# Optimization experiments

Measured on AMD Instinct MI355X. Metric: run time of the kernel, lower is better.

## Reference

```python
import jax, jax.numpy as jnp
import numpy as np
import math

B, T, C, H, D = 2, 2048, 768, 12, 64


def _rms_norm(x):
    # torch F.rms_norm with eps=None -> finfo(dtype).eps, no learned weight
    eps = jnp.finfo(x.dtype).eps
    return x * jax.lax.rsqrt(jnp.mean(x * x, axis=-1, keepdims=True) + eps)


def _apply_rotary(x, cos, sin):
    # nanochat rotary: split head_dim into halves
    d = x.shape[-1] // 2
    x1, x2 = x[..., :d], x[..., d:]
    return jnp.concatenate([x1 * cos + x2 * sin, -x1 * sin + x2 * cos], axis=-1)


def setup_inputs() -> dict:
    key = jax.random.key(0)
    ks = jax.random.split(key, 8)
    s = 0.02
    x = jax.random.normal(ks[0], (B, T, C), jnp.float32)
    cos = jax.random.normal(ks[1], (1, T, 1, D // 2), jnp.float32)
    sin = jax.random.normal(ks[2], (1, T, 1, D // 2), jnp.float32)
    Wq = jax.random.normal(ks[3], (C, C), jnp.float32) * s
    Wk = jax.random.normal(ks[4], (C, C), jnp.float32) * s
    Wv = jax.random.normal(ks[5], (C, C), jnp.float32) * s
    Wo = jax.random.normal(ks[6], (C, C), jnp.float32) * s
    beta = jnp.ones((H,), jnp.float32) * 0.5
    return {"x": x, "cos": cos, "sin": sin, "Wq": Wq, "Wk": Wk, "Wv": Wv, "Wo": Wo, "beta": beta}


def reference(x, cos, sin, Wq, Wk, Wv, Wo, beta):
    b, t, c = x.shape
    h = beta.shape[0]
    d = c // h
    q = (x @ Wq.T).reshape(b, t, h, d)
    k = (x @ Wk.T).reshape(b, t, h, d)
    v = (x @ Wv.T).reshape(b, t, h, d)
    q = _rms_norm(_apply_rotary(q, cos, sin)).transpose(0, 2, 1, 3)  # (B,H,T,D)
    k = _rms_norm(_apply_rotary(k, cos, sin)).transpose(0, 2, 1, 3)
    v = v.transpose(0, 2, 1, 3)
    # phase coherence: mean over RoPE frequencies of cos(position_diff * theta)
    pos = jnp.arange(t, dtype=jnp.float32)
    theta = 10000.0 ** (-jnp.arange(0, d, 2, dtype=jnp.float32) / d)  # (D/2,)
    pdiff = pos[None, :] - pos[:, None]  # (T,T); cos is even so orientation is irrelevant
    coh_base = jnp.mean(jnp.cos(pdiff[:, :, None] * theta), axis=-1)  # (T,T)
    coherence = 1.0 + beta[None, :, None, None] * coh_base[None, None, :, :]  # (1,H,T,T)
    scores = jnp.einsum('bhqd,bhkd->bhqk', q, k) / math.sqrt(d)
    scores = scores * coherence
    w = jax.nn.softmax(scores, axis=-1)
    causal = jnp.tril(jnp.ones((t, t), dtype=bool))
    w = w * causal[None, None, :, :]
    w = w / (jnp.sum(w, axis=-1, keepdims=True) + 1e-8)
    y = jnp.einsum('bhqk,bhkd->bhqd', w, v)
    y = y.transpose(0, 2, 1, 3).reshape(b, t, c)
    return y @ Wo.T
```

## Files before the change

### kernel.cpp

```cpp
#include <hip/hip_runtime.h>
#include <hip/hip_bf16.h>
#include <math.h>

#define B_ 2
#define T_ 2048
#define C_ 768
#define H_ 12
#define D_ 64

typedef __attribute__((ext_vector_type(8))) short short8;
typedef __attribute__((ext_vector_type(4))) float f32x4;
typedef __attribute__((ext_vector_type(16))) float f32x16;

template <bool V> struct BoolC { static constexpr bool value = V; };

#define SBAR() do { asm volatile("" ::: "memory"); __builtin_amdgcn_s_barrier(); asm volatile("" ::: "memory"); } while (0)
#define WAITVM(N) asm volatile("s_waitcnt vmcnt(" #N ")" ::: "memory")

__device__ inline unsigned short f2bf(float f) {
    unsigned int x = __float_as_uint(f);
    unsigned int r = x + 0x7FFFu + ((x >> 16) & 1u);
    return (unsigned short)(r >> 16);
}

__device__ __forceinline__ unsigned cvtpk(float lo, float hi) {
    unsigned r;
    asm("v_cvt_pk_bf16_f32 %0, %1, %2" : "=v"(r) : "v"(lo), "v"(hi));
    return r;
}

__device__ __forceinline__ void plswap(unsigned& a, unsigned& b) {
    asm volatile("v_permlane32_swap_b32 %0, %1" : "+v"(a), "+v"(b));
}

__device__ __forceinline__ void gll16(const void* g, void* l) {
    __builtin_amdgcn_global_load_lds(
        (const __attribute__((address_space(1))) unsigned int*)g,
        (__attribute__((address_space(3))) unsigned int*)l, 16, 0, 0);
}

__global__ __launch_bounds__(256) void convert_all_kernel(const float* __restrict__ x,
                                                          const float* __restrict__ Wq,
                                                          const float* __restrict__ Wk,
                                                          const float* __restrict__ Wv,
                                                          const float* __restrict__ Wo,
                                                          unsigned short* __restrict__ xb,
                                                          unsigned short* __restrict__ wqkv,
                                                          unsigned short* __restrict__ wob,
                                                          float* __restrict__ coh) {
    if (blockIdx.x >= 5376) {
        int dd = (blockIdx.x - 5376) * 256 + threadIdx.x;
        if (dd < T_) {
            float s = 0.f;
            for (int m = 0; m < 32; ++m) {
                float theta = powf(10000.f, -(float)m / 32.f);
                s += cosf((float)dd * theta);
            }
            coh[dd] = s * (1.f / 32.f);
        }
        return;
    }
    int i = blockIdx.x * 256 + threadIdx.x;
    float4 v;
    ushort4* d;
    if (i < 786432) {
        v = ((const float4*)x)[i];
        d = (ushort4*)xb + i;
    } else {
        int wI = i - 786432;
        int widx = wI / 147456;
        int off = wI - widx * 147456;
        const float* W = widx == 0 ? Wq : widx == 1 ? Wk : widx == 2 ? Wv : Wo;
        v = ((const float4*)W)[off];
        unsigned short* base = (widx == 3) ? wob : (wqkv + widx * 589824);
        d = (ushort4*)base + off;
    }
    ushort4 o;
    o.x = f2bf(v.x); o.y = f2bf(v.y); o.z = f2bf(v.z); o.w = f2bf(v.w);
    *d = o;
}

union QkvSmem {
    struct { unsigned short A[2][128][32]; unsigned short Bm[2][64][32]; } g;
    unsigned short tr[64][136];
};

__global__ __launch_bounds__(256, 4) void gemm_qkv_kernel(const unsigned short* __restrict__ xb,
                                                          const unsigned short* __restrict__ wqkv,
                                                          const float* __restrict__ cosb,
                                                          const float* __restrict__ sinb,
                                                          unsigned short* __restrict__ qbf,
                                                          unsigned short* __restrict__ kbf,
                                                          unsigned short* __restrict__ vt) {
    __shared__ QkvSmem sm;

    int bm = blockIdx.x, tn = blockIdx.y;
    int tid = threadIdx.x;
    int w = tid >> 6, lane = tid & 63;
    int rc = lane & 15, kg = lane >> 4;

    const unsigned short* ga = xb + (size_t)(bm * 128 + w * 32 + (lane >> 2)) * 768 + (lane & 3) * 8;
    const unsigned short* gb = wqkv + (size_t)(tn * 64 + w * 16 + (lane >> 2)) * 768 + (lane & 3) * 8;

    f32x4 acc[2][4];
    #pragma unroll
    for (int i = 0; i < 2; ++i)
        #pragma unroll
        for (int j = 0; j < 4; ++j) acc[i][j] = (f32x4){0.f, 0.f, 0.f, 0.f};

    auto stageg = [&](int buf, int k0) {
        gll16(ga + k0, &sm.g.A[buf][w * 32][0]);
        gll16(ga + k0 + 16 * 768, &sm.g.A[buf][w * 32 + 16][0]);
        gll16(gb + k0, &sm.g.Bm[buf][w * 16][0]);
    };
    auto comp = [&](int buf) {
        short8 aF[2], bF[4];
        #pragma unroll
        for (int ai = 0; ai < 2; ++ai) aF[ai] = *(const short8*)&sm.g.A[buf][w * 32 + ai * 16 + rc][kg * 8];
        #pragma unroll
        for (int bj = 0; bj < 4; ++bj) bF[bj] = *(const short8*)&sm.g.Bm[buf][bj * 16 + rc][kg * 8];
        __builtin_amdgcn_s_setprio(1);
        #pragma unroll
        for (int ai = 0; ai < 2; ++ai)
            #pragma unroll
            for (int bj = 0; bj < 4; ++bj)
                acc[ai][bj] = __builtin_amdgcn_mfma_f32_16x16x32_bf16(aF[ai], bF[bj], acc[ai][bj], 0, 0, 0);
        __builtin_amdgcn_s_setprio(0);
    };

    stageg(0, 0);
    __syncthreads();
    for (int kk = 0; kk < 23; ++kk) {
        stageg((kk + 1) & 1, (kk + 1) * 32);
        WAITVM(3);
        SBAR();
        comp(kk & 1);
        SBAR();
    }
    WAITVM(0);
    SBAR();
    comp(1);
    __syncthreads();

    int tensor = tn / 12;
    int h = tn % 12;

    if (tensor < 2) {
        float scale = tensor == 0 ? 0.125f : 1.0f;
        unsigned short* dst = (tensor == 0 ? qbf : kbf);
        #pragma unroll
        for (int ai = 0; ai < 2; ++ai) {
            #pragma unroll
            for (int rr = 0; rr < 4; ++rr) {
                int m = bm * 128 + w * 32 + ai * 16 + kg * 4 + rr;
                int b = m >> 11, t = m & 2047;
                float c0 = cosb[t * 32 + rc], c1 = cosb[t * 32 + 16 + rc];
                float s0 = sinb[t * 32 + rc], s1 = sinb[t * 32 + 16 + rc];
                float x0 = acc[ai][0][rr], x1 = acc[ai][1][rr];
                float x2 = acc[ai][2][rr], x3 = acc[ai][3][rr];
                float o0 = x0 * c0 + x2 * s0;
                float o1 = x1 * c1 + x3 * s1;
                float o2 = -x0 * s0 + x2 * c0;
                float o3 = -x1 * s1 + x3 * c1;
                float ss = o0 * o0 + o1 * o1 + o2 * o2 + o3 * o3;
                ss += __shfl_xor(ss, 1); ss += __shfl_xor(ss, 2);
                ss += __shfl_xor(ss, 4); ss += __shfl_xor(ss, 8);
                float rn = rsqrtf(ss * (1.f / 64.f) + 1.1920929e-07f) * scale;
                unsigned short* dp = dst + (((size_t)b * H_ + h) * T_ + t) * 64;
                dp[rc]      = f2bf(o0 * rn);
                dp[16 + rc] = f2bf(o1 * rn);
                dp[32 + rc] = f2bf(o2 * rn);
                dp[48 + rc] = f2bf(o3 * rn);
            }
        }
    } else {
        #pragma unroll
        for (int ai = 0; ai < 2; ++ai)
            #pragma unroll
            for (int bj = 0; bj < 4; ++bj)
                #pragma unroll
                for (int rr = 0; rr < 4; ++rr)
                    sm.tr[bj * 16 + rc][w * 32 + ai * 16 + kg * 4 + rr] = f2bf(acc[ai][bj][rr]);
        __syncthreads();
        int m0 = bm * 128;
        int b = m0 >> 11, t0 = m0 & 2047;
        int d = w * 16 + (lane >> 2);
        int tl = (lane & 3) * 32;
        unsigned short* gp = vt + (((size_t)b * H_ + h) * 64 + d) * T_ + t0 + tl;
        #pragma unroll
        for (int i = 0; i < 4; ++i)
            *(uint4*)(gp + i * 8) = *(const uint4*)&sm.tr[d][tl + i * 8];
    }
}

__global__ __launch_bounds__(256, 4) void gemm_out_kernel(const unsigned short* __restrict__ A,
                                                          const unsigned short* __restrict__ Bw,
                                                          float* __restrict__ C) {
    __shared__ unsigned short lA[2][64][32];
    __shared__ unsigned short lB[2][64][32];
    int bm = blockIdx.x, tn = blockIdx.y;
    int tid = threadIdx.x;
    int w = tid >> 6, lane = tid & 63;
    int rc = lane & 15, kg = lane >> 4;
    int wr = w >> 1, wc = w & 1;

    const unsigned short* ga = A + (size_t)(bm * 64 + w * 16 + (lane >> 2)) * 768 + (lane & 3) * 8;
    const unsigned short* gbB = Bw + (size_t)(tn * 64 + w * 16 + (lane >> 2)) * 768 + (lane & 3) * 8;

    f32x4 acc[2][2];
    #pragma unroll
    for (int i = 0; i < 2; ++i)
        #pragma unroll
        for (int j = 0; j < 2; ++j) acc[i][j] = (f32x4){0.f, 0.f, 0.f, 0.f};

    auto stageg = [&](int buf, int k0) {
        gll16(ga + k0, &lA[buf][w * 16][0]);
        gll16(gbB + k0, &lB[buf][w * 16][0]);
    };
    auto comp = [&](int buf) {
        short8 aF[2], bF[2];
        #pragma unroll
        for (int ai = 0; ai < 2; ++ai) aF[ai] = *(const short8*)&lA[buf][wr * 32 + ai * 16 + rc][kg * 8];
        #pragma unroll
        for (int bj = 0; bj < 2; ++bj) bF[bj] = *(const short8*)&lB[buf][wc * 32 + bj * 16 + rc][kg * 8];
        __builtin_amdgcn_s_setprio(1);
        #pragma unroll
        for (int ai = 0; ai < 2; ++ai)
            #pragma unroll
            for (int bj = 0; bj < 2; ++bj)
                acc[ai][bj] = __builtin_amdgcn_mfma_f32_16x16x32_bf16(aF[ai], bF[bj], acc[ai][bj], 0, 0, 0);
        __builtin_amdgcn_s_setprio(0);
    };

    stageg(0, 0);
    __syncthreads();
    for (int kk = 0; kk < 23; ++kk) {
        stageg((kk + 1) & 1, (kk + 1) * 32);
        WAITVM(2);
        SBAR();
        comp(kk & 1);
        SBAR();
    }
    WAITVM(0);
    SBAR();
    comp(1);

    #pragma unroll
    for (int ai = 0; ai < 2; ++ai)
        #pragma unroll
        for (int rr = 0; rr < 4; ++rr) {
            int m = bm * 64 + wr * 32 + ai * 16 + kg * 4 + rr;
            #pragma unroll
            for (int bj = 0; bj < 2; ++bj)
                C[(size_t)m * 768 + tn * 64 + wc * 32 + bj * 16 + rc] = acc[ai][bj][rr];
        }
}

__global__ __launch_bounds__(256, 4) void attn_flash_kernel(const unsigned short* __restrict__ qbf,
                                                            const unsigned short* __restrict__ kbf,
                                                            const unsigned short* __restrict__ vt,
                                                            const float* __restrict__ coh,
                                                            const float* __restrict__ beta,
                                                            unsigned short* __restrict__ yb) {
    __shared__ unsigned short kT[2][64][64];
    __shared__ unsigned short vT[2][64][64];
    __shared__ float cfl[T_];

    int p = blockIdx.x;
    int xcd = p & 7, kk = p >> 3;
    int bl = kk >> 5, jsl = kk & 31;
    int bh = xcd * 3 + bl;
    int jj = (bl == 0) ? jsl : (bl == 1 ? (31 - jsl) : ((jsl * 5 + 3) & 31));
    int tq = 31 - jj;
    int b = bh / H_, h = bh % H_;

    int tid = threadIdx.x;
    int w = tid >> 6, lane = tid & 63;
    int qs = w >> 1, js = w & 1;
    int ql = lane & 31, hl = lane >> 5;

    float bv = beta[h];
    for (int i = tid; i < T_; i += 256)
        cfl[i] = (1.f + bv * coh[i]) * 1.4426950408889634f;

    int qb = tq * 64;
    const unsigned short* kb = kbf + (size_t)bh * T_ * 64;
    const unsigned short* vb = vt + (size_t)bh * 64 * T_;

    const unsigned short* qrow = qbf + ((size_t)bh * T_ + qb + qs * 32 + ql) * 64 + hl * 8;
    short8 qf[4];
    #pragma unroll
    for (int d = 0; d < 4; ++d) qf[d] = *(const short8*)(qrow + d * 16);

    f32x16 acc0, acc1;
    #pragma unroll
    for (int i = 0; i < 16; ++i) { acc0[i] = 0.f; acc1[i] = 0.f; }
    float z = 0.f;

    int Rk = js * 32 + ql;
    int kby[4];
    #pragma unroll
    for (int d = 0; d < 4; ++d) kby[d] = Rk * 128 + (((d * 2 + hl) ^ (Rk & 7)) << 4);
    int vby0[2], vby1[2];
    #pragma unroll
    for (int ks = 0; ks < 2; ++ks) {
        int Rv0 = ql, Rv1 = 32 + ql;
        vby0[ks] = Rv0 * 128 + (((js * 4 + ks * 2 + hl) ^ (Rv0 & 7)) << 4);
        vby1[ks] = Rv1 * 128 + (((js * 4 + ks * 2 + hl) ^ (Rv1 & 7)) << 4);
    }
    const char* kbase = (const char*)&kT[0][0][0];
    const char* vbase = (const char*)&vT[0][0][0];

    int rloc = lane >> 3;
    int gsw = ((lane & 7) ^ rloc) * 8;
    int r0 = w * 16;

    auto stage = [&](int buf, int tj) {
        gll16(kb + (size_t)(tj + r0 + rloc) * 64 + gsw,      &kT[buf][r0][0]);
        gll16(kb + (size_t)(tj + r0 + 8 + rloc) * 64 + gsw,  &kT[buf][r0 + 8][0]);
        gll16(vb + (size_t)(r0 + rloc) * T_ + tj + gsw,      &vT[buf][r0][0]);
        gll16(vb + (size_t)(r0 + 8 + rloc) * T_ + tj + gsw,  &vT[buf][r0 + 8][0]);
    };

    int qpos = qb + qs * 32 + ql;

    auto body = [&](int buf, int tj, auto maskc) {
        constexpr bool M = decltype(maskc)::value;
        f32x16 s;
        #pragma unroll
        for (int i = 0; i < 16; ++i) s[i] = 0.f;
        const char* kp = kbase + buf * 8192;
        __builtin_amdgcn_s_setprio(1);
        #pragma unroll
        for (int d = 0; d < 4; ++d) {
            short8 kf = *(const short8*)(kp + kby[d]);
            s = __builtin_amdgcn_mfma_f32_32x32x16_bf16(kf, qf[d], s, 0, 0, 0);
        }
        __builtin_amdgcn_s_setprio(0);
        int base = qpos - tj - js * 32 - 4 * hl;
        float e[16];
        #pragma unroll
        for (int r = 0; r < 16; ++r) {
            int dd = base - ((r & 3) + 8 * (r >> 2));
            if constexpr (M) {
                float ex = __builtin_amdgcn_exp2f(s[r] * cfl[dd < 0 ? 0 : dd]);
                e[r] = dd >= 0 ? ex : 0.f;
            } else {
                e[r] = __builtin_amdgcn_exp2f(s[r] * cfl[dd]);
            }
            z += e[r];
        }
        unsigned A0 = cvtpk(e[0], e[1]),  B0 = cvtpk(e[2], e[3]);
        unsigned C0 = cvtpk(e[4], e[5]),  D0 = cvtpk(e[6], e[7]);
        unsigned E0 = cvtpk(e[8], e[9]),  F0 = cvtpk(e[10], e[11]);
        unsigned G0 = cvtpk(e[12], e[13]), H0 = cvtpk(e[14], e[15]);
        plswap(A0, C0); plswap(B0, D0); plswap(E0, G0); plswap(F0, H0);
        union U { unsigned u[4]; short8 s8; };
        U p0, p1;
        p0.u[0] = A0; p0.u[1] = B0; p0.u[2] = C0; p0.u[3] = D0;
        p1.u[0] = E0; p1.u[1] = F0; p1.u[2] = G0; p1.u[3] = H0;
        const char* vp = vbase + buf * 8192;
        short8 v00 = *(const short8*)(vp + vby0[0]);
        short8 v01 = *(const short8*)(vp + vby0[1]);
        short8 v10 = *(const short8*)(vp + vby1[0]);
        short8 v11 = *(const short8*)(vp + vby1[1]);
        __builtin_amdgcn_s_setprio(1);
        acc0 = __builtin_amdgcn_mfma_f32_32x32x16_bf16(v00, p0.s8, acc0, 0, 0, 0);
        acc0 = __builtin_amdgcn_mfma_f32_32x32x16_bf16(v01, p1.s8, acc0, 0, 0, 0);
        acc1 = __builtin_amdgcn_mfma_f32_32x32x16_bf16(v10, p0.s8, acc1, 0, 0, 0);
        acc1 = __builtin_amdgcn_mfma_f32_32x32x16_bf16(v11, p1.s8, acc1, 0, 0, 0);
        __builtin_amdgcn_s_setprio(0);
    };

    int nt = tq + 1;
    stage(0, 0);
    __syncthreads();
    int cur = 0;
    for (int it = 0; it < nt - 1; ++it) {
        stage(cur ^ 1, (it + 1) * 64);
        WAITVM(4);
        SBAR();
        body(cur, it * 64, BoolC<false>{});
        SBAR();
        cur ^= 1;
    }
    WAITVM(0);
    SBAR();
    if (qs > js)      body(cur, (nt - 1) * 64, BoolC<false>{});
    else if (qs == js) body(cur, (nt - 1) * 64, BoolC<true>{});
    __syncthreads();

    z += __shfl_xor(z, 32);
    float* osc = (float*)&kT[0][0][0];
    float* zbuf = (float*)&vT[0][0][0];
    if (js == 0) {
        float* o = osc + qs * 2048;
        #pragma unroll
        for (int r = 0; r < 16; ++r) {
            o[r * 64 + lane] = acc0[r];
            o[(16 + r) * 64 + lane] = acc1[r];
        }
        if (lane < 32) zbuf[qs * 32 + ql] = z;
    }
    __syncthreads();
    if (js == 1) {
        float zt = z + zbuf[qs * 32 + ql];
        float invz = 1.f / zt;
        const float* o = osc + qs * 2048;
        #pragma unroll
        for (int r = 0; r < 16; ++r) {
            acc0[r] = (acc0[r] + o[r * 64 + lane]) * invz;
            acc1[r] = (acc1[r] + o[(16 + r) * 64 + lane]) * invz;
        }
        int t = qb + qs * 32 + ql;
        unsigned short* yp = yb + (((size_t)b * T_ + t) * H_ + h) * 64;
        #pragma unroll
        for (int g = 0; g < 4; ++g) {
            uint2 st0, st1;
            st0.x = cvtpk(acc0[g * 4 + 0], acc0[g * 4 + 1]);
            st0.y = cvtpk(acc0[g * 4 + 2], acc0[g * 4 + 3]);
            *(uint2*)(yp + g * 8 + 4 * hl) = st0;
            st1.x = cvtpk(acc1[g * 4 + 0], acc1[g * 4 + 1]);
            st1.y = cvtpk(acc1[g * 4 + 2], acc1[g * 4 + 3]);
            *(uint2*)(yp + 32 + g * 8 + 4 * hl) = st1;
        }
    }
}

extern "C" void kernel_launch(void* const* d_in, const int* in_sizes, int n_in,
                              void* d_out, int out_size, void* d_ws, size_t ws_size,
                              hipStream_t stream) {
    const float* x    = (const float*)d_in[0];
    const float* cosb = (const float*)d_in[1];
    const float* sinb = (const float*)d_in[2];
    const float* Wq   = (const float*)d_in[3];
    const float* Wk   = (const float*)d_in[4];
    const float* Wv   = (const float*)d_in[5];
    const float* Wo   = (const float*)d_in[6];
    const float* beta = (const float*)d_in[7];
    float* out = (float*)d_out;

    char* ws = (char*)d_ws;
    unsigned short* xb   = (unsigned short*)(ws + 0);
    unsigned short* wqkv = (unsigned short*)(ws + 6291456);
    unsigned short* wob  = (unsigned short*)(ws + 9830400);
    unsigned short* qbf  = (unsigned short*)(ws + 11010048);
    unsigned short* kbf  = (unsigned short*)(ws + 17301504);
    unsigned short* vt   = (unsigned short*)(ws + 23592960);
    unsigned short* yb   = (unsigned short*)(ws + 29884416);
    float*          coh  = (float*)(ws + 36175872);

    convert_all_kernel<<<5384, 256, 0, stream>>>(x, Wq, Wk, Wv, Wo, xb, wqkv, wob, coh);

    dim3 gq(32, 36);
    gemm_qkv_kernel<<<gq, 256, 0, stream>>>(xb, wqkv, cosb, sinb, qbf, kbf, vt);

    attn_flash_kernel<<<B_ * H_ * (T_ / 64), 256, 0, stream>>>(qbf, kbf, vt, coh, beta, yb);

    dim3 go(64, 12);
    gemm_out_kernel<<<go, 256, 0, stream>>>(yb, wob, out);
}
```

Baseline: 98.01 us.

## Precompute per-head coherence scale table globally and read it from global memory in attention

The per-head scaled coherence table (1+beta*coh)*log2e is now computed once per head in the convert kernel, instead of being rebuilt into shared memory by every attention block. The attention kernel drops its 8KB shared array and the prologue loop, and instead loads the 16 coefficients per tile directly from global memory (cached), issued before the exp loop. Occupancy hint lowered from 4 to 3 waves per SIMD. The cost is extra global/L1 loads in the inner loop and possibly lower occupancy; the gain is shorter block startup and less LDS usage.

```diff
diff --git a/kernel.cpp b/kernel.cpp
--- a/kernel.cpp
+++ b/kernel.cpp
@@ -44,20 +44,22 @@
                                                           const float* __restrict__ Wk,
                                                           const float* __restrict__ Wv,
                                                           const float* __restrict__ Wo,
+                                                          const float* __restrict__ beta,
                                                           unsigned short* __restrict__ xb,
                                                           unsigned short* __restrict__ wqkv,
                                                           unsigned short* __restrict__ wob,
-                                                          float* __restrict__ coh) {
+                                                          float* __restrict__ cflg) {
     if (blockIdx.x >= 5376) {
-        int dd = (blockIdx.x - 5376) * 256 + threadIdx.x;
-        if (dd < T_) {
-            float s = 0.f;
-            for (int m = 0; m < 32; ++m) {
-                float theta = powf(10000.f, -(float)m / 32.f);
-                s += cosf((float)dd * theta);
-            }
-            coh[dd] = s * (1.f / 32.f);
-        }
+        int idx = (blockIdx.x - 5376) * 256 + threadIdx.x;
+        int h = idx >> 11;
+        int dd = idx & 2047;
+        float s = 0.f;
+        for (int m = 0; m < 32; ++m) {
+            float theta = powf(10000.f, -(float)m / 32.f);
+            s += cosf((float)dd * theta);
+        }
+        s *= (1.f / 32.f);
+        cflg[idx] = (1.f + beta[h] * s) * 1.4426950408889634f;
         return;
     }
     int i = blockIdx.x * 256 + threadIdx.x;
@@ -256,15 +258,13 @@
         }
 }
 
-__global__ __launch_bounds__(256, 4) void attn_flash_kernel(const unsigned short* __restrict__ qbf,
+__global__ __launch_bounds__(256, 3) void attn_flash_kernel(const unsigned short* __restrict__ qbf,
                                                             const unsigned short* __restrict__ kbf,
                                                             const unsigned short* __restrict__ vt,
-                                                            const float* __restrict__ coh,
-                                                            const float* __restrict__ beta,
+                                                            const float* __restrict__ cflg,
                                                             unsigned short* __restrict__ yb) {
     __shared__ unsigned short kT[2][64][64];
     __shared__ unsigned short vT[2][64][64];
-    __shared__ float cfl[T_];
 
     int p = blockIdx.x;
     int xcd = p & 7, kk = p >> 3;
@@ -279,9 +279,7 @@
     int qs = w >> 1, js = w & 1;
     int ql = lane & 31, hl = lane >> 5;
 
-    float bv = beta[h];
-    for (int i = tid; i < T_; i += 256)
-        cfl[i] = (1.f + bv * coh[i]) * 1.4426950408889634f;
+    const float* cflh = cflg + (h << 11);
 
     int qb = tq * 64;
     const unsigned short* kb = kbf + (size_t)bh * T_ * 64;
@@ -338,17 +336,22 @@
         }
         __builtin_amdgcn_s_setprio(0);
         int base = qpos - tj - js * 32 - 4 * hl;
-        float e[16];
+        float cv[16];
         #pragma unroll
         for (int r = 0; r < 16; ++r) {
             int dd = base - ((r & 3) + 8 * (r >> 2));
+            cv[r] = cflh[M ? (dd < 0 ? 0 : dd) : dd];
+        }
+        float e[16];
+        #pragma unroll
+        for (int r = 0; r < 16; ++r) {
+            float ex = __builtin_amdgcn_exp2f(s[r] * cv[r]);
             if constexpr (M) {
-                float ex = __builtin_amdgcn_exp2f(s[r] * cfl[dd < 0 ? 0 : dd]);
-                e[r] = dd >= 0 ? ex : 0.f;
-            } else {
-                e[r] = __builtin_amdgcn_exp2f(s[r] * cfl[dd]);
+                int dd = base - ((r & 3) + 8 * (r >> 2));
+                ex = dd >= 0 ? ex : 0.f;
             }
-            z += e[r];
+            e[r] = ex;
+            z += ex;
         }
         unsigned A0 = cvtpk(e[0], e[1]),  B0 = cvtpk(e[2], e[3]);
         unsigned C0 = cvtpk(e[4], e[5]),  D0 = cvtpk(e[6], e[7]);
@@ -448,14 +451,14 @@
     unsigned short* kbf  = (unsigned short*)(ws + 17301504);
     unsigned short* vt   = (unsigned short*)(ws + 23592960);
     unsigned short* yb   = (unsigned short*)(ws + 29884416);
-    float*          coh  = (float*)(ws + 36175872);
-
-    convert_all_kernel<<<5384, 256, 0, stream>>>(x, Wq, Wk, Wv, Wo, xb, wqkv, wob, coh);
+    float*          cflg = (float*)(ws + 36175872);
+
+    convert_all_kernel<<<5472, 256, 0, stream>>>(x, Wq, Wk, Wv, Wo, beta, xb, wqkv, wob, cflg);
 
     dim3 gq(32, 36);
     gemm_qkv_kernel<<<gq, 256, 0, stream>>>(xb, wqkv, cosb, sinb, qbf, kbf, vt);
 
-    attn_flash_kernel<<<B_ * H_ * (T_ / 64), 256, 0, stream>>>(qbf, kbf, vt, coh, beta, yb);
+    attn_flash_kernel<<<B_ * H_ * (T_ / 64), 256, 0, stream>>>(qbf, kbf, vt, cflg, yb);
 
     dim3 go(64, 12);
     gemm_out_kernel<<<go, 256, 0, stream>>>(yb, wob, out);
```

Result: slower. 111.3 us (+13.5%).
